# Performance work log

Measured on AMD Instinct MI355X. Metric: run time of the kernel, lower is better.

The kernel has to match this reference:

```python
import jax, jax.numpy as jnp
import numpy as np

N, S, B, C = 8192, 13, 2, 3
EPS = 1e-6
LAMBDA_COORD, LAMBDA_OBJ, LAMBDA_NOOBJ, LAMBDA_CLASS = 5.0, 1.0, 0.5, 1.0


def setup_inputs() -> dict:
    key = jax.random.key(0)
    k1, k2, k3, k4 = jax.random.split(key, 4)
    predictions = jax.random.normal(k1, (N, S, S, B * (5 + C)), dtype=jnp.float32)
    xywh = jax.random.uniform(k2, (N, S, S, 4), dtype=jnp.float32)
    conf = (jax.random.uniform(k3, (N, S, S)) < 0.3).astype(jnp.float32)  # binary objectness
    cls_idx = jax.random.randint(k4, (N, S, S), 0, C)
    onehot = jax.nn.one_hot(cls_idx, C, dtype=jnp.float32)
    targets = jnp.concatenate(
        [xywh, conf[..., None], jnp.zeros((N, S, S, 5), jnp.float32), onehot], axis=-1
    )  # (N,S,S,13)
    return {"predictions": predictions, "targets": targets}


def reference(predictions, targets):
    batch = predictions.shape[0]
    mask = targets[..., 4] > 0  # (N,S,S) object-present mask
    m = mask.astype(predictions.dtype)

    # --- coord loss (box 0 only, as in the torch loop) ---
    px = jax.nn.sigmoid(predictions[..., 0])
    py = jax.nn.sigmoid(predictions[..., 1])
    pw, ph = predictions[..., 2], predictions[..., 3]
    tx, ty, tw, th = (targets[..., k] for k in range(4))
    coord = (
        (px - tx) ** 2
        + (py - ty) ** 2
        + (jnp.sqrt(jnp.abs(pw) + EPS) - jnp.sqrt(jnp.abs(tw) + EPS)) ** 2
        + (jnp.sqrt(jnp.abs(ph) + EPS) - jnp.sqrt(jnp.abs(th) + EPS)) ** 2
    )
    coord_loss = jnp.sum(m * coord)

    # --- objectness BCE (box 0) on object cells ---
    z = predictions[..., 4]
    tc = targets[..., 4]
    bce_obj = -(tc * jax.nn.log_sigmoid(z) + (1.0 - tc) * jax.nn.log_sigmoid(-z))
    conf_loss_obj = jnp.sum(m * bce_obj)

    # --- no-object BCE on both boxes (target 0) ---
    z_all = predictions[..., jnp.array([4, 9])]  # (N,S,S,B) conf logits
    bce_noobj = -jax.nn.log_sigmoid(-z_all)  # BCE(sigmoid(z), 0)
    conf_loss_noobj = jnp.sum((1.0 - m)[..., None] * bce_noobj)

    # --- class CE on object cells ---
    logits = predictions[..., B * 5 : B * 5 + C]  # (N,S,S,C)
    tcls = jnp.argmax(targets[..., B * 5 : B * 5 + C], axis=-1)
    ce = jax.nn.logsumexp(logits, axis=-1) - jnp.take_along_axis(
        logits, tcls[..., None], axis=-1
    )[..., 0]
    class_loss = jnp.sum(m * ce)

    # normalize by batch only if any such cell exists (matches torch branching)
    n_obj = jnp.sum(mask)
    n_noobj = mask.size - n_obj
    div_obj = jnp.where(n_obj > 0, 1.0 / batch, 1.0)
    div_noobj = jnp.where(n_noobj > 0, 1.0 / batch, 1.0)

    total = (
        LAMBDA_COORD * coord_loss * div_obj
        + LAMBDA_OBJ * conf_loss_obj * div_obj
        + LAMBDA_NOOBJ * conf_loss_noobj * div_noobj
        + LAMBDA_CLASS * class_loss * div_obj
    )
    return total
```

## Files before the change

kernel.cpp:

```cpp
#include <hip/hip_runtime.h>
#include <math.h>


#define EPSV 1e-6f

__global__ __launch_bounds__(256) void phobia_partial(
    const float* __restrict__ pred, const float* __restrict__ tgt,
    float* __restrict__ ws, long long cells)
{
    long long idx0 = (long long)blockIdx.x * blockDim.x + threadIdx.x;
    long long stride = (long long)gridDim.x * blockDim.x;

    float accA = 0.f;
    float accB = 0.f;
    float accC = 0.f;

    for (long long i = idx0; i < cells; i += stride) {
        const float* pr = pred + i * 16;
        const float* tr = tgt  + i * 13;

        float4 p03   = *reinterpret_cast<const float4*>(pr);
        float  p4    = pr[4];
        float  p9    = pr[9];
        float2 p1011 = *reinterpret_cast<const float2*>(pr + 10);
        float  p12   = pr[12];

        float t0 = tr[0], t1 = tr[1], t2 = tr[2], t3 = tr[3], t4 = tr[4];
        float t10 = tr[10], t11 = tr[11], t12 = tr[12];

        float m = (t4 > 0.f) ? 1.f : 0.f;

        float px = 1.f / (1.f + expf(-p03.x));
        float py = 1.f / (1.f + expf(-p03.y));
        float dx = px - t0;
        float dy = py - t1;
        float dw = sqrtf(fabsf(p03.z) + EPSV) - sqrtf(fabsf(t2) + EPSV);
        float dh = sqrtf(fabsf(p03.w) + EPSV) - sqrtf(fabsf(t3) + EPSV);
        float coord = dx*dx + dy*dy + dw*dw + dh*dh;

        float l1p4 = log1pf(expf(-fabsf(p4)));
        float logsig_p4 = fminf(p4, 0.f) - l1p4;
        float logsig_m4 = fminf(-p4, 0.f) - l1p4;
        float bce_obj = -(t4 * logsig_p4 + (1.f - t4) * logsig_m4);
        float bce_no4 = -logsig_m4;
        float bce_no9 = fmaxf(p9, 0.f) + log1pf(expf(-fabsf(p9)));

        int tcls = 0; float bt = t10;
        if (t11 > bt) { bt = t11; tcls = 1; }
        if (t12 > bt) { tcls = 2; }
        float lt = (tcls == 0) ? p1011.x : ((tcls == 1) ? p1011.y : p12);
        float mx = fmaxf(p1011.x, fmaxf(p1011.y, p12));
        float lse = mx + logf(expf(p1011.x - mx) + expf(p1011.y - mx) + expf(p12 - mx));
        float ce = lse - lt;

        accA += m * (5.f * coord + bce_obj + ce);
        accB += (1.f - m) * (bce_no4 + bce_no9);
        accC += m;
    }

    #pragma unroll
    for (int o = 32; o > 0; o >>= 1) {
        accA += __shfl_down(accA, o, 64);
        accB += __shfl_down(accB, o, 64);
        accC += __shfl_down(accC, o, 64);
    }
    __shared__ float sA[4], sB[4], sC[4];
    int wave = threadIdx.x >> 6;
    int lane = threadIdx.x & 63;
    if (lane == 0) { sA[wave] = accA; sB[wave] = accB; sC[wave] = accC; }
    __syncthreads();
    if (threadIdx.x == 0) {
        float A = sA[0] + sA[1] + sA[2] + sA[3];
        float B = sB[0] + sB[1] + sB[2] + sB[3];
        float C = sC[0] + sC[1] + sC[2] + sC[3];
        ws[blockIdx.x * 3 + 0] = A;
        ws[blockIdx.x * 3 + 1] = B;
        ws[blockIdx.x * 3 + 2] = C;
    }
}

__global__ __launch_bounds__(1024) void phobia_final(
    const float* __restrict__ ws, int nblocks, float* __restrict__ out, long long cells)
{
    float a = 0.f, b = 0.f, c = 0.f;
    for (int i = threadIdx.x; i < nblocks; i += 1024) {
        a += ws[i * 3 + 0];
        b += ws[i * 3 + 1];
        c += ws[i * 3 + 2];
    }
    #pragma unroll
    for (int o = 32; o > 0; o >>= 1) {
        a += __shfl_down(a, o, 64);
        b += __shfl_down(b, o, 64);
        c += __shfl_down(c, o, 64);
    }
    __shared__ float sA[16], sB[16], sC[16];
    int wave = threadIdx.x >> 6;
    int lane = threadIdx.x & 63;
    if (lane == 0) { sA[wave] = a; sB[wave] = b; sC[wave] = c; }
    __syncthreads();
    if (threadIdx.x == 0) {
        float A = 0.f, B = 0.f, C = 0.f;
        #pragma unroll
        for (int w = 0; w < 16; ++w) { A += sA[w]; B += sB[w]; C += sC[w]; }
        float batch = (float)(cells / 169);
        float invb = 1.f / batch;
        float div_obj   = (C > 0.f) ? invb : 1.f;
        float div_noobj = (C < (float)cells) ? invb : 1.f;
        out[0] = A * div_obj + 0.5f * B * div_noobj;
    }
}

extern "C" void kernel_launch(void* const* d_in, const int* in_sizes, int n_in,
                              void* d_out, int out_size, void* d_ws, size_t ws_size,
                              hipStream_t stream) {
    const float* pred = (const float*)d_in[0];
    const float* tgt  = (const float*)d_in[1];
    float* out = (float*)d_out;
    float* ws  = (float*)d_ws;

    long long cells = (long long)in_sizes[0] / 16;

    int blocks = 1024;
    size_t need = (size_t)blocks * 3 * sizeof(float);
    while (need > ws_size && blocks > 1) { blocks >>= 1; need = (size_t)blocks * 3 * sizeof(float); }

    phobia_partial<<<blocks, 256, 0, stream>>>(pred, tgt, ws, cells);
    phobia_final<<<1, 1024, 0, stream>>>(ws, blocks, out, cells);
}
```

Baseline: 34.39 us.

## Process two cells per thread, size grid to data, use fast intrinsics

```diff
diff --git a/kernel.cpp b/kernel.cpp
--- a/kernel.cpp
+++ b/kernel.cpp
@@ -4,58 +4,74 @@
 
 #define EPSV 1e-6f
 
+struct CellIn {
+    float4 p03; float p4, p9, p10, p11, p12;
+    float t0, t1, t2, t3, t4, t10, t11, t12;
+};
+
+__device__ __forceinline__ void load_cell(const float* __restrict__ pred,
+                                          const float* __restrict__ tgt,
+                                          long long i, CellIn& c) {
+    const float* pr = pred + i * 16;
+    const float* tr = tgt  + i * 13;
+    c.p03 = *reinterpret_cast<const float4*>(pr);
+    c.p4  = pr[4];
+    c.p9  = pr[9];
+    float2 p1011 = *reinterpret_cast<const float2*>(pr + 10);
+    c.p10 = p1011.x; c.p11 = p1011.y;
+    c.p12 = pr[12];
+    c.t0 = tr[0]; c.t1 = tr[1]; c.t2 = tr[2]; c.t3 = tr[3]; c.t4 = tr[4];
+    c.t10 = tr[10]; c.t11 = tr[11]; c.t12 = tr[12];
+}
+
+__device__ __forceinline__ void accum_cell(const CellIn& c, float& accA, float& accB, float& accC) {
+    float m = (c.t4 > 0.f) ? 1.f : 0.f;
+
+    float px = 1.f / (1.f + __expf(-c.p03.x));
+    float py = 1.f / (1.f + __expf(-c.p03.y));
+    float dx = px - c.t0;
+    float dy = py - c.t1;
+    float dw = sqrtf(fabsf(c.p03.z) + EPSV) - sqrtf(fabsf(c.t2) + EPSV);
+    float dh = sqrtf(fabsf(c.p03.w) + EPSV) - sqrtf(fabsf(c.t3) + EPSV);
+    float coord = dx*dx + dy*dy + dw*dw + dh*dh;
+
+    float l1p4 = __logf(1.f + __expf(-fabsf(c.p4)));
+    float logsig_p4 = fminf(c.p4, 0.f) - l1p4;
+    float logsig_m4 = fminf(-c.p4, 0.f) - l1p4;
+    float bce_obj = -(c.t4 * logsig_p4 + (1.f - c.t4) * logsig_m4);
+    float bce_no4 = -logsig_m4;
+    float bce_no9 = fmaxf(c.p9, 0.f) + __logf(1.f + __expf(-fabsf(c.p9)));
+
+    int tcls = 0; float bt = c.t10;
+    if (c.t11 > bt) { bt = c.t11; tcls = 1; }
+    if (c.t12 > bt) { tcls = 2; }
+    float lt = (tcls == 0) ? c.p10 : ((tcls == 1) ? c.p11 : c.p12);
+    float mx = fmaxf(c.p10, fmaxf(c.p11, c.p12));
+    float lse = mx + __logf(__expf(c.p10 - mx) + __expf(c.p11 - mx) + __expf(c.p12 - mx));
+    float ce = lse - lt;
+
+    accA += m * (5.f * coord + bce_obj + ce);
+    accB += (1.f - m) * (bce_no4 + bce_no9);
+    accC += m;
+}
+
 __global__ __launch_bounds__(256) void phobia_partial(
     const float* __restrict__ pred, const float* __restrict__ tgt,
-    float* __restrict__ ws, long long cells)
+    float* __restrict__ ws, long long cells, long long half)
 {
     long long idx0 = (long long)blockIdx.x * blockDim.x + threadIdx.x;
     long long stride = (long long)gridDim.x * blockDim.x;
 
-    float accA = 0.f;
-    float accB = 0.f;
-    float accC = 0.f;
+    float accA = 0.f, accB = 0.f, accC = 0.f;
 
-    for (long long i = idx0; i < cells; i += stride) {
-        const float* pr = pred + i * 16;
-        const float* tr = tgt  + i * 13;
-
-        float4 p03   = *reinterpret_cast<const float4*>(pr);
-        float  p4    = pr[4];
-        float  p9    = pr[9];
-        float2 p1011 = *reinterpret_cast<const float2*>(pr + 10);
-        float  p12   = pr[12];
-
-        float t0 = tr[0], t1 = tr[1], t2 = tr[2], t3 = tr[3], t4 = tr[4];
-        float t10 = tr[10], t11 = tr[11], t12 = tr[12];
-
-        float m = (t4 > 0.f) ? 1.f : 0.f;
-
-        float px = 1.f / (1.f + expf(-p03.x));
-        float py = 1.f / (1.f + expf(-p03.y));
-        float dx = px - t0;
-        float dy = py - t1;
-        float dw = sqrtf(fabsf(p03.z) + EPSV) - sqrtf(fabsf(t2) + EPSV);
-        float dh = sqrtf(fabsf(p03.w) + EPSV) - sqrtf(fabsf(t3) + EPSV);
-        float coord = dx*dx + dy*dy + dw*dw + dh*dh;
-
-        float l1p4 = log1pf(expf(-fabsf(p4)));
-        float logsig_p4 = fminf(p4, 0.f) - l1p4;
-        float logsig_m4 = fminf(-p4, 0.f) - l1p4;
-        float bce_obj = -(t4 * logsig_p4 + (1.f - t4) * logsig_m4);
-        float bce_no4 = -logsig_m4;
-        float bce_no9 = fmaxf(p9, 0.f) + log1pf(expf(-fabsf(p9)));
-
-        int tcls = 0; float bt = t10;
-        if (t11 > bt) { bt = t11; tcls = 1; }
-        if (t12 > bt) { tcls = 2; }
-        float lt = (tcls == 0) ? p1011.x : ((tcls == 1) ? p1011.y : p12);
-        float mx = fmaxf(p1011.x, fmaxf(p1011.y, p12));
-        float lse = mx + logf(expf(p1011.x - mx) + expf(p1011.y - mx) + expf(p12 - mx));
-        float ce = lse - lt;
-
-        accA += m * (5.f * coord + bce_obj + ce);
-        accB += (1.f - m) * (bce_no4 + bce_no9);
-        accC += m;
+    for (long long i = idx0; i < half; i += stride) {
+        long long j = i + half;
+        CellIn c0, c1;
+        bool have1 = (j < cells);
+        load_cell(pred, tgt, i, c0);
+        if (have1) load_cell(pred, tgt, j, c1);
+        accum_cell(c0, accA, accB, accC);
+        if (have1) accum_cell(c1, accA, accB, accC);
     }
 
     #pragma unroll
@@ -70,12 +86,9 @@
     if (lane == 0) { sA[wave] = accA; sB[wave] = accB; sC[wave] = accC; }
     __syncthreads();
     if (threadIdx.x == 0) {
-        float A = sA[0] + sA[1] + sA[2] + sA[3];
-        float B = sB[0] + sB[1] + sB[2] + sB[3];
-        float C = sC[0] + sC[1] + sC[2] + sC[3];
-        ws[blockIdx.x * 3 + 0] = A;
-        ws[blockIdx.x * 3 + 1] = B;
-        ws[blockIdx.x * 3 + 2] = C;
+        ws[blockIdx.x * 3 + 0] = sA[0] + sA[1] + sA[2] + sA[3];
+        ws[blockIdx.x * 3 + 1] = sB[0] + sB[1] + sB[2] + sB[3];
+        ws[blockIdx.x * 3 + 2] = sC[0] + sC[1] + sC[2] + sC[3];
     }
 }
 
@@ -120,11 +133,12 @@
     float* ws  = (float*)d_ws;
 
     long long cells = (long long)in_sizes[0] / 16;
+    long long half  = (cells + 1) / 2;
 
-    int blocks = 1024;
+    int blocks = (int)((half + 255) / 256);
     size_t need = (size_t)blocks * 3 * sizeof(float);
     while (need > ws_size && blocks > 1) { blocks >>= 1; need = (size_t)blocks * 3 * sizeof(float); }
 
-    phobia_partial<<<blocks, 256, 0, stream>>>(pred, tgt, ws, cells);
+    phobia_partial<<<blocks, 256, 0, stream>>>(pred, tgt, ws, cells, half);
     phobia_final<<<1, 1024, 0, stream>>>(ws, blocks, out, cells);
 }
```

Result: slower. 51.53 us (+49.9%).
